# Performance work log

Measured on AMD Instinct MI355X. Metric: run time of the kernel, lower is better.

## Reference

```python
import jax, jax.numpy as jnp
import numpy as np

B, S, D = 16, 1024, 512
N_LAYERS = 3


def setup_inputs() -> dict:
    key = jax.random.key(0)
    ks = jax.random.split(key, 8)
    sc = 0.02  # small init scale keeps gates in a sane range
    return {
        "inputs": jax.random.normal(ks[0], (B, S, D), jnp.float32),
        "h0": jax.random.normal(ks[1], (N_LAYERS, B, D), jnp.float32),
        # GRU params, PyTorch layout: gates ordered (r, z, n), weight [3D, D]
        "w_ih": jax.random.normal(ks[2], (N_LAYERS, 3 * D, D), jnp.float32) * sc,
        "w_hh": jax.random.normal(ks[3], (N_LAYERS, 3 * D, D), jnp.float32) * sc,
        "b_ih": jnp.zeros((N_LAYERS, 3 * D), jnp.float32),
        "b_hh": jnp.zeros((N_LAYERS, 3 * D), jnp.float32),
        "ln0_g": jnp.ones((D,), jnp.float32),
        "ln0_b": jnp.zeros((D,), jnp.float32),
        "ln1_g": jnp.ones((D,), jnp.float32),
        "ln1_b": jnp.zeros((D,), jnp.float32),
        "w1": jax.random.normal(ks[4], (D, 4 * D), jnp.float32) * sc,
        "b1": jnp.zeros((4 * D,), jnp.float32),
        "w2": jax.random.normal(ks[5], (4 * D, D), jnp.float32) * sc,
        "b2": jnp.zeros((D,), jnp.float32),
    }


def _layer_norm(x, g, b, eps=1e-5):
    mu = jnp.mean(x, axis=-1, keepdims=True)
    var = jnp.var(x, axis=-1, keepdims=True)
    return (x - mu) * jax.lax.rsqrt(var + eps) * g + b


def _gru_stack(x, h0, w_ih, w_hh, b_ih, b_hh):
    # x: [S, B, D] time-major; PyTorch GRU math, gate order (r, z, n).
    for l in range(N_LAYERS):
        # precompute input projections for all timesteps (batched GEMM)
        gi = jnp.einsum('sbd,gd->sbg', x, w_ih[l]) + b_ih[l]  # [S, B, 3D]
        w_hh_l_T = w_hh[l].T
        b_hh_l = b_hh[l]

        def step(h, gi_t):
            gh = h @ w_hh_l_T + b_hh_l                       # [B, 3D]
            i_r, i_z, i_n = jnp.split(gi_t, 3, axis=-1)
            h_r, h_z, h_n = jnp.split(gh, 3, axis=-1)
            r = jax.nn.sigmoid(i_r + h_r)
            z = jax.nn.sigmoid(i_z + h_z)
            n = jnp.tanh(i_n + r * h_n)
            h_new = (1.0 - z) * n + z * h
            return h_new, h_new

        _, x = jax.lax.scan(step, h0[l], gi)                 # x: [S, B, D]
    return x


def reference(inputs, h0, w_ih, w_hh, b_ih, b_hh,
              ln0_g, ln0_b, ln1_g, ln1_b, w1, b1, w2, b2):
    # inputs: [B, S, D] -> time-major [S, B, D]
    x = _layer_norm(jnp.transpose(inputs, (1, 0, 2)), ln0_g, ln0_b)
    h = _gru_stack(x, h0, w_ih, w_hh, b_ih, b_hh)            # [S, B, D]
    out = inputs + jnp.transpose(h, (1, 0, 2))               # residual 1 (dropout=identity, eval)
    y = _layer_norm(out, ln1_g, ln1_b)
    ffn = jax.nn.gelu(y @ w1 + b1, approximate=False) @ w2 + b2
    return out + ffn                                          # residual 2
```

## Files before the change

kernel.cpp:

```cpp
#include <hip/hip_runtime.h>
#include <hip/hip_bf16.h>

typedef unsigned short u16;
typedef unsigned int   u32;
typedef unsigned long long u64;
typedef __attribute__((ext_vector_type(8))) short short8;
typedef __attribute__((ext_vector_type(4))) float f32x4;

__device__ __forceinline__ float bf2f(u16 u) {
  union { u32 i; float f; } v; v.i = ((u32)u) << 16; return v.f;
}
__device__ __forceinline__ u16 f2bf(float f) {
  union { float f; u32 i; } v; v.f = f;
  return (u16)((v.i + 0x7FFFu + ((v.i >> 16) & 1u)) >> 16);
}

typedef const __attribute__((address_space(1))) u32* gas_t;
typedef __attribute__((address_space(3)))       u32* las_t;
__device__ __forceinline__ void gld16(const void* g, void* l) {
  __builtin_amdgcn_global_load_lds((gas_t)g, (las_t)l, 16, 0, 0);
}

__global__ __launch_bounds__(256) void cast_kernel(const float* __restrict__ src,
                                                   u16* __restrict__ dst, int n) {
  int i = (blockIdx.x * 256 + threadIdx.x) * 4;
  if (i >= n) return;
  float4 v = *(const float4*)(src + i);
  uint2 o;
  o.x = (u32)f2bf(v.x) | ((u32)f2bf(v.y) << 16);
  o.y = (u32)f2bf(v.z) | ((u32)f2bf(v.w) << 16);
  *(uint2*)(dst + i) = o;
}

__global__ __launch_bounds__(256) void tcast_kernel(const float* __restrict__ src,
                                                    u16* __restrict__ dst, int R, int C) {
  __shared__ u16 tile[32][33];
  int c0 = blockIdx.x * 32, r0 = blockIdx.y * 32;
  for (int dy = threadIdx.y; dy < 32; dy += 8)
    tile[dy][threadIdx.x] = f2bf(src[(size_t)(r0 + dy) * C + c0 + threadIdx.x]);
  __syncthreads();
  for (int dy = threadIdx.y; dy < 32; dy += 8)
    dst[(size_t)(c0 + dy) * R + r0 + threadIdx.x] = tile[threadIdx.x][dy];
}

__global__ __launch_bounds__(256) void hprep_kernel(const float* __restrict__ h0,
                                                    u64* __restrict__ hbuf) {
  int l = blockIdx.x;
  const float* h = h0 + l * 8192;
  u64* buf = hbuf + (size_t)l * 2 * 4096;
  for (int idx = threadIdx.x; idx < 4096; idx += 256) {
    int row = idx >> 8, wl = idx & 255;
    int d0 = wl * 2;
    u64 p0 = f2bf(h[row * 512 + d0]);
    u64 p1 = f2bf(h[row * 512 + d0 + 1]);
    buf[idx] = p0 | (p1 << 32);
  }
}

__global__ __launch_bounds__(256) void ln0_kernel(const float* __restrict__ in,
                                                  const float* __restrict__ g,
                                                  const float* __restrict__ be,
                                                  u16* __restrict__ xout) {
  int m = blockIdx.x;
  int b = m >> 10, s = m & 1023;
  int i = threadIdx.x * 2;
  float2 v = *(const float2*)(in + (size_t)m * 512 + i);
  float sum = v.x + v.y, sq = v.x * v.x + v.y * v.y;
  for (int o = 32; o > 0; o >>= 1) { sum += __shfl_down(sum, o); sq += __shfl_down(sq, o); }
  __shared__ float red[10];
  int w = threadIdx.x >> 6, lane = threadIdx.x & 63;
  if (!lane) { red[w] = sum; red[w + 4] = sq; }
  __syncthreads();
  if (threadIdx.x == 0) {
    sum = red[0] + red[1] + red[2] + red[3];
    sq  = red[4] + red[5] + red[6] + red[7];
    float mu = sum * (1.f / 512.f), var = sq * (1.f / 512.f) - mu * mu;
    red[8] = mu; red[9] = rsqrtf(var + 1e-5f);
  }
  __syncthreads();
  float mu = red[8], rs = red[9];
  u32 o0 = (u32)f2bf((v.x - mu) * rs * g[i] + be[i]) |
           ((u32)f2bf((v.y - mu) * rs * g[i + 1] + be[i + 1]) << 16);
  *(u32*)(xout + (size_t)(s * 16 + b) * 512 + i) = o0;
}

__global__ __launch_bounds__(256) void resid_ln1_kernel(const float* __restrict__ in,
                                                        const u16* __restrict__ hrec,
                                                        const float* __restrict__ g,
                                                        const float* __restrict__ be,
                                                        float* __restrict__ outf,
                                                        u16* __restrict__ y) {
  int m = blockIdx.x;
  int b = m >> 10, s = m & 1023;
  int i = threadIdx.x * 2;
  float2 v = *(const float2*)(in + (size_t)m * 512 + i);
  u32 hu = *(const u32*)(hrec + (size_t)(s * 16 + b) * 512 + i);
  v.x += bf2f((u16)(hu & 0xffff));
  v.y += bf2f((u16)(hu >> 16));
  *(float2*)(outf + (size_t)m * 512 + i) = v;
  float sum = v.x + v.y, sq = v.x * v.x + v.y * v.y;
  for (int o = 32; o > 0; o >>= 1) { sum += __shfl_down(sum, o); sq += __shfl_down(sq, o); }
  __shared__ float red[10];
  int w = threadIdx.x >> 6, lane = threadIdx.x & 63;
  if (!lane) { red[w] = sum; red[w + 4] = sq; }
  __syncthreads();
  if (threadIdx.x == 0) {
    sum = red[0] + red[1] + red[2] + red[3];
    sq  = red[4] + red[5] + red[6] + red[7];
    float mu = sum * (1.f / 512.f), var = sq * (1.f / 512.f) - mu * mu;
    red[8] = mu; red[9] = rsqrtf(var + 1e-5f);
  }
  __syncthreads();
  float mu = red[8], rs = red[9];
  u32 o0 = (u32)f2bf((v.x - mu) * rs * g[i] + be[i]) |
           ((u32)f2bf((v.y - mu) * rs * g[i + 1] + be[i + 1]) << 16);
  *(u32*)(y + (size_t)m * 512 + i) = o0;
}

template <int EPI>
__global__ __launch_bounds__(256, 2)
void gemm_bt(const u16* __restrict__ A, const u16* __restrict__ Bt,
             void* __restrict__ Out, const float* __restrict__ bias,
             const float* __restrict__ resid, int M, int N, int K) {
  __shared__ u16 As[128 * 64];
  __shared__ u16 Bs[128 * 64];
  const int bn = blockIdx.x, bm = blockIdx.y;
  const int tid = threadIdx.x;
  const int w = tid >> 6, lane = tid & 63;
  const int wr = w >> 1, wc = w & 1;
  const int col = lane & 15, kg = lane >> 4;
  const int l8 = lane >> 3, l7 = lane & 7;
  f32x4 acc[4][4];
#pragma unroll
  for (int i = 0; i < 4; ++i)
#pragma unroll
    for (int j = 0; j < 4; ++j) acc[i][j] = (f32x4){0.f, 0.f, 0.f, 0.f};

  for (int k0 = 0; k0 < K; k0 += 64) {
    __syncthreads();
#pragma unroll
    for (int i = 0; i < 4; ++i) {
      int q = w * 4 + i;
      int row = q * 8 + l8;
      int cswz = (l7 * 16) ^ ((row & 7) << 4);
      gld16((const char*)A + ((size_t)(bm * 128 + row) * K + k0) * 2 + cswz,
            (char*)As + q * 1024);
      gld16((const char*)Bt + ((size_t)(bn * 128 + row) * K + k0) * 2 + cswz,
            (char*)Bs + q * 1024);
    }
    asm volatile("s_waitcnt vmcnt(0)" ::: "memory");
    __syncthreads();
#pragma unroll
    for (int kc = 0; kc < 2; ++kc) {
      short8 af[4], bfr[4];
      int cb = kc * 64 + kg * 16;
#pragma unroll
      for (int mi = 0; mi < 4; ++mi) {
        int r = wr * 64 + mi * 16 + col;
        af[mi] = *(const short8*)((const char*)As + r * 128 + (cb ^ ((r & 7) << 4)));
      }
#pragma unroll
      for (int ni = 0; ni < 4; ++ni) {
        int r = wc * 64 + ni * 16 + col;
        bfr[ni] = *(const short8*)((const char*)Bs + r * 128 + (cb ^ ((r & 7) << 4)));
      }
#pragma unroll
      for (int mi = 0; mi < 4; ++mi)
#pragma unroll
        for (int ni = 0; ni < 4; ++ni)
          acc[mi][ni] = __builtin_amdgcn_mfma_f32_16x16x32_bf16(af[mi], bfr[ni], acc[mi][ni], 0, 0, 0);
    }
  }
#pragma unroll
  for (int ni = 0; ni < 4; ++ni) {
    int gn = bn * 128 + wc * 64 + ni * 16 + col;
    float bv = bias ? bias[gn] : 0.f;
#pragma unroll
    for (int mi = 0; mi < 4; ++mi) {
      int gmb = bm * 128 + wr * 64 + mi * 16 + kg * 4;
#pragma unroll
      for (int j = 0; j < 4; ++j) {
        float v = acc[mi][ni][j] + bv;
        size_t idx = (size_t)(gmb + j) * N + gn;
        if (EPI == 0) {
          ((u16*)Out)[idx] = f2bf(v);
        } else if (EPI == 1) {
          float gel = 0.5f * v * (1.f + erff(v * 0.7071067811865476f));
          ((u16*)Out)[idx] = f2bf(gel);
        } else {
          ((float*)Out)[idx] = v + resid[idx];
        }
      }
    }
  }
}

__device__ __forceinline__ void gather_poll(const u64* __restrict__ plane, u32 want,
                                            int w, int lane, u16* __restrict__ lds) {
  const u64 TM = 0xFFFF0000FFFF0000ULL;
  const u64 ex = ((u64)want << 16) | ((u64)want << 48);
  u64 v[16];
#pragma unroll
  for (int r = 0; r < 4; ++r)
#pragma unroll
    for (int q = 0; q < 4; ++q)
      v[r * 4 + q] = __hip_atomic_load(plane + (size_t)(w * 4 + r) * 256 + lane * 4 + q,
                                       __ATOMIC_RELAXED, __HIP_MEMORY_SCOPE_AGENT);
  for (;;) {
    bool ok = true;
#pragma unroll
    for (int i = 0; i < 16; ++i) ok &= ((v[i] ^ ex) & TM) == 0;
    if (ok) break;
    __builtin_amdgcn_s_sleep(1);
#pragma unroll
    for (int i = 0; i < 16; ++i)
      if (((v[i] ^ ex) & TM) != 0)
        v[i] = __hip_atomic_load(plane + (size_t)(w * 4 + (i >> 2)) * 256 + lane * 4 + (i & 3),
                                 __ATOMIC_RELAXED, __HIP_MEMORY_SCOPE_AGENT);
  }
#pragma unroll
  for (int r = 0; r < 4; ++r) {
    int row = w * 4 + r;
    uint4 pk;
    pk.x = ((u32)v[r * 4 + 0] & 0xFFFFu) | ((u32)(v[r * 4 + 0] >> 32) << 16);
    pk.y = ((u32)v[r * 4 + 1] & 0xFFFFu) | ((u32)(v[r * 4 + 1] >> 32) << 16);
    pk.z = ((u32)v[r * 4 + 2] & 0xFFFFu) | ((u32)(v[r * 4 + 2] >> 32) << 16);
    pk.w = ((u32)v[r * 4 + 3] & 0xFFFFu) | ((u32)(v[r * 4 + 3] >> 32) << 16);
    *(uint4*)((char*)lds + row * 1024 + ((lane * 16) ^ ((row & 7) << 4))) = pk;
  }
}

__global__ __launch_bounds__(256, 1)
void rec3_kernel(const u16* __restrict__ gib, const u16* __restrict__ whhb,
                 const u16* __restrict__ wihb, const float* __restrict__ bih,
                 const float* __restrict__ bhh, const float* __restrict__ h0,
                 u64* __restrict__ hpl, u64* __restrict__ xr,
                 u64* __restrict__ gip, u16* __restrict__ xout) {
  const int res = blockIdx.x & 7, grp = blockIdx.x >> 3;
  if (res > 4) return;
  __shared__ u16 hs[16 * 512];
  const int tid = threadIdx.x;
  const int w = tid >> 6, lane = tid & 63;
  const int col = lane & 15, kg = lane >> 4;
  const u64 TM = 0xFFFF0000FFFF0000ULL;

  if (res >= 3) {
    const int l = res - 2, k = grp;
    const int d = k * 64 + w * 16 + col;
    const u16* wih = wihb + (size_t)l * 1536 * 512;
    short8 wi0[16], wi1[16], wi2[16];
    {
      const u16* r0 = wih + (size_t)(0 * 512 + d) * 512;
      const u16* r1 = wih + (size_t)(1 * 512 + d) * 512;
      const u16* r2 = wih + (size_t)(2 * 512 + d) * 512;
#pragma unroll
      for (int kc = 0; kc < 16; ++kc) {
        wi0[kc] = *(const short8*)(r0 + kc * 32 + kg * 8);
        wi1[kc] = *(const short8*)(r1 + kc * 32 + kg * 8);
        wi2[kc] = *(const short8*)(r2 + kc * 32 + kg * 8);
      }
    }
    const float bi0 = bih[l * 1536 + d], bi1 = bih[l * 1536 + 512 + d],
                bi2 = bih[l * 1536 + 1024 + d];
    const u64* upx = xr + (size_t)(l - 1) * 8 * 4096;
    u64* gout = gip + (size_t)(l - 1) * 4 * 12288;
    const u64* hpc = hpl + (size_t)l * 2 * 4096;
    u64 bpv = 0;

    for (int t = 1; t <= 1024; ++t) {
      gather_poll(upx + (size_t)(t & 7) * 4096, (u32)t, w, lane, hs);
      __syncthreads();
      f32x4 ar = {0.f, 0.f, 0.f, 0.f}, az = ar, an = ar;
#pragma unroll
      for (int kc = 0; kc < 16; ++kc) {
        int cb = kc * 64 + kg * 16;
        short8 a = *(const short8*)((const char*)hs + col * 1024 + (cb ^ ((col & 7) << 4)));
        ar = __builtin_amdgcn_mfma_f32_16x16x32_bf16(a, wi0[kc], ar, 0, 0, 0);
        az = __builtin_amdgcn_mfma_f32_16x16x32_bf16(a, wi1[kc], az, 0, 0, 0);
        an = __builtin_amdgcn_mfma_f32_16x16x32_bf16(a, wi2[kc], an, 0, 0, 0);
      }
      if (t > 4) {
        u32 need = (u32)(t - 4);
        u32 ctag = (u32)(bpv >> 16) & 0xFFFFu;
        while (ctag < need) {
          __builtin_amdgcn_s_sleep(8);
          bpv = __hip_atomic_load(hpc + (size_t)(need & 1) * 4096 + k * 32,
                                  __ATOMIC_RELAXED, __HIP_MEMORY_SCOPE_AGENT);
          ctag = (u32)(bpv >> 16) & 0xFFFFu;
        }
      }
      {
        const u32 tgl = (u32)t << 16;
        u64* slot = gout + (size_t)(t & 3) * 12288 + (size_t)k * 1536;
#pragma unroll
        for (int g = 0; g < 3; ++g) {
          f32x4 a = (g == 0) ? ar : ((g == 1) ? az : an);
          float bg = (g == 0) ? bi0 : ((g == 1) ? bi1 : bi2);
#pragma unroll
          for (int jh = 0; jh < 2; ++jh) {
            u32 lo = (u32)f2bf(a[2 * jh] + bg) | tgl;
            u32 hi = (u32)f2bf(a[2 * jh + 1] + bg) | tgl;
            __hip_atomic_store(slot + (size_t)(g * 64 + w * 16 + col) * 8 + kg * 2 + jh,
                               (u64)lo | ((u64)hi << 32),
                               __ATOMIC_RELAXED, __HIP_MEMORY_SCOPE_AGENT);
          }
        }
      }
      if (t >= 4)
        bpv = __hip_atomic_load(hpc + (size_t)((t - 3) & 1) * 4096 + k * 32,
                                __ATOMIC_RELAXED, __HIP_MEMORY_SCOPE_AGENT);
      __syncthreads();
    }
    return;
  }

  const int l = res, blk = grp;
  const int d = blk * 64 + w * 16 + col;
  const u16* whh = whhb + (size_t)l * 1536 * 512;
  short8 wh0[16], wh1[16], wh2[16];
  {
    const u16* r0 = whh + (size_t)(0 * 512 + d) * 512;
    const u16* r1 = whh + (size_t)(1 * 512 + d) * 512;
    const u16* r2 = whh + (size_t)(2 * 512 + d) * 512;
#pragma unroll
    for (int kc = 0; kc < 16; ++kc) {
      wh0[kc] = *(const short8*)(r0 + kc * 32 + kg * 8);
      wh1[kc] = *(const short8*)(r1 + kc * 32 + kg * 8);
      wh2[kc] = *(const short8*)(r2 + kc * 32 + kg * 8);
    }
  }
  const float bh0 = bhh[l * 1536 + d], bh1 = bhh[l * 1536 + 512 + d],
              bh2 = bhh[l * 1536 + 1024 + d];
  float hprev[4];
#pragma unroll
  for (int j = 0; j < 4; ++j) hprev[j] = h0[l * 8192 + (kg * 4 + j) * 512 + d];

  u64* ownp = hpl + (size_t)l * 2 * 4096;
  u64* dnx = xr + (size_t)l * 8 * 4096;
  const u64* gin = gip + (size_t)(l - 1) * 4 * 12288;
  const u64* gchk = gip + (size_t)l * 4 * 12288;
  const bool ev = !(col & 1);
  u64 bp8 = 0;

  for (int t = 1; t <= 1024; ++t) {
    float gir[3][4];
    u64 gv[6];
    if (l == 0) {
#pragma unroll
      for (int gte = 0; gte < 3; ++gte)
#pragma unroll
        for (int j = 0; j < 4; ++j)
          gir[gte][j] = bf2f(gib[((size_t)(t - 1) * 16 + kg * 4 + j) * 1536 + gte * 512 + d]);
    } else {
      const u64* gs = gin + (size_t)(t & 3) * 12288 + (size_t)blk * 1536;
#pragma unroll
      for (int g = 0; g < 3; ++g)
#pragma unroll
        for (int jh = 0; jh < 2; ++jh)
          gv[g * 2 + jh] = __hip_atomic_load(gs + (size_t)(g * 64 + w * 16 + col) * 8 + kg * 2 + jh,
                                             __ATOMIC_RELAXED, __HIP_MEMORY_SCOPE_AGENT);
    }

    gather_poll(ownp + (size_t)((t - 1) & 1) * 4096, (u32)(t - 1), w, lane, hs);

    if (l > 0) {
      const u64 exg = ((u64)t << 16) | ((u64)t << 48);
      const u64* gs = gin + (size_t)(t & 3) * 12288 + (size_t)blk * 1536;
      for (;;) {
        bool ok = true;
#pragma unroll
        for (int i = 0; i < 6; ++i) ok &= ((gv[i] ^ exg) & TM) == 0;
        if (ok) break;
        __builtin_amdgcn_s_sleep(1);
#pragma unroll
        for (int g = 0; g < 3; ++g)
#pragma unroll
          for (int jh = 0; jh < 2; ++jh)
            if (((gv[g * 2 + jh] ^ exg) & TM) != 0)
              gv[g * 2 + jh] = __hip_atomic_load(gs + (size_t)(g * 64 + w * 16 + col) * 8 + kg * 2 + jh,
                                                 __ATOMIC_RELAXED, __HIP_MEMORY_SCOPE_AGENT);
      }
#pragma unroll
      for (int g = 0; g < 3; ++g)
#pragma unroll
        for (int jh = 0; jh < 2; ++jh) {
          gir[g][2 * jh]     = bf2f((u16)gv[g * 2 + jh]);
          gir[g][2 * jh + 1] = bf2f((u16)(gv[g * 2 + jh] >> 32));
        }
    }
    __syncthreads();

    f32x4 ar = {0.f, 0.f, 0.f, 0.f}, az = ar, an = ar;
#pragma unroll
    for (int kc = 0; kc < 16; ++kc) {
      int cb = kc * 64 + kg * 16;
      short8 a = *(const short8*)((const char*)hs + col * 1024 + (cb ^ ((col & 7) << 4)));
      ar = __builtin_amdgcn_mfma_f32_16x16x32_bf16(a, wh0[kc], ar, 0, 0, 0);
      az = __builtin_amdgcn_mfma_f32_16x16x32_bf16(a, wh1[kc], az, 0, 0, 0);
      an = __builtin_amdgcn_mfma_f32_16x16x32_bf16(a, wh2[kc], an, 0, 0, 0);
    }
    u32 po[4];
#pragma unroll
    for (int j = 0; j < 4; ++j) {
      float rg = 1.f / (1.f + expf(-(gir[0][j] + ar[j] + bh0)));
      float zg = 1.f / (1.f + expf(-(gir[1][j] + az[j] + bh1)));
      float ng = tanhf(gir[2][j] + rg * (an[j] + bh2));
      float hn = (1.f - zg) * ng + zg * hprev[j];
      hprev[j] = hn;
      po[j] = (u32)f2bf(hn);
    }

    {
      const u32 tg = (u32)t << 16;
      u32 pn[4];
#pragma unroll
      for (int j = 0; j < 4; ++j) pn[j] = (u32)__shfl_xor((int)po[j], 1);
      int j0 = ev ? 0 : 2;
      u64 wd[2]; int wi_[2];
#pragma unroll
      for (int jj = 0; jj < 2; ++jj) {
        int j = j0 + jj;
        u32 lo = (ev ? po[j] : pn[j]) | tg;
        u32 hi = (ev ? pn[j] : po[j]) | tg;
        int row = kg * 4 + j;
        wd[jj] = (u64)lo | ((u64)hi << 32);
        wi_[jj] = row * 256 + blk * 32 + w * 8 + (col >> 1);
      }
      u64* op = ownp + (size_t)(t & 1) * 4096;
#pragma unroll
      for (int jj = 0; jj < 2; ++jj)
        __hip_atomic_store(op + wi_[jj], wd[jj], __ATOMIC_RELAXED, __HIP_MEMORY_SCOPE_AGENT);

      if (l < 2) {
        if (t > 8) {
          u32 need = (u32)(t - 8);
          for (;;) {
            u32 tg8 = (lane < 8) ? (u32)((bp8 >> 16) & 0xFFFFu) : 0xFFFFu;
            if (__all(tg8 >= need)) break;
            __builtin_amdgcn_s_sleep(8);
            if (lane < 8)
              bp8 = __hip_atomic_load(gchk + (size_t)(need & 3) * 12288 + (size_t)lane * 1536,
                                      __ATOMIC_RELAXED, __HIP_MEMORY_SCOPE_AGENT);
          }
        }
        u64* xp = dnx + (size_t)(t & 7) * 4096;
#pragma unroll
        for (int jj = 0; jj < 2; ++jj)
          __hip_atomic_store(xp + wi_[jj], wd[jj], __ATOMIC_RELAXED, __HIP_MEMORY_SCOPE_AGENT);
        if (t >= 8 && lane < 8)
          bp8 = __hip_atomic_load(gchk + (size_t)((t - 7) & 3) * 12288 + (size_t)lane * 1536,
                                  __ATOMIC_RELAXED, __HIP_MEMORY_SCOPE_AGENT);
      } else {
        u32 pr[4], qr[4];
#pragma unroll
        for (int j = 0; j < 4; ++j) {
          pr[j] = ev ? (po[j] | (pn[j] << 16)) : (pn[j] | (po[j] << 16));
          qr[j] = (u32)__shfl_xor((int)pr[j], 2);
        }
        int jx = col & 3;
        u64 raw = ((col & 2) == 0) ? ((u64)pr[jx] | ((u64)qr[jx] << 32))
                                   : ((u64)qr[jx] | ((u64)pr[jx] << 32));
        int row = kg * 4 + jx;
        *(u64*)(xout + ((size_t)(t - 1) * 16 + row) * 512 + blk * 64 + w * 16 + (col & ~3)) = raw;
      }
    }
    __syncthreads();
  }
}

extern "C" void kernel_launch(void* const* d_in, const int* in_sizes, int n_in,
                              void* d_out, int out_size, void* d_ws, size_t ws_size,
                              hipStream_t stream) {
  const float* inp = (const float*)d_in[0];
  const float* h0  = (const float*)d_in[1];
  const float* wih = (const float*)d_in[2];
  const float* whh = (const float*)d_in[3];
  const float* bih = (const float*)d_in[4];
  const float* bhh = (const float*)d_in[5];
  const float* g0  = (const float*)d_in[6];
  const float* be0 = (const float*)d_in[7];
  const float* g1  = (const float*)d_in[8];
  const float* be1 = (const float*)d_in[9];
  const float* w1  = (const float*)d_in[10];
  const float* b1  = (const float*)d_in[11];
  const float* w2  = (const float*)d_in[12];
  const float* b2  = (const float*)d_in[13];
  float* out = (float*)d_out;

  char* p = (char*)d_ws;
  auto alloc = [&](size_t bytes) {
    char* r = p;
    p += (bytes + 255) & ~(size_t)255;
    return r;
  };
  u16* xa    = (u16*)alloc(16384ull * 512 * 2);
  u16* xb    = (u16*)alloc(16384ull * 512 * 2);
  u16* gib   = (u16*)alloc(16384ull * 1536 * 2);
  u16* mid   = (u16*)alloc(16384ull * 2048 * 2);
  float* outf = (float*)alloc(16384ull * 512 * 4);
  u16* wihb  = (u16*)alloc(3ull * 1536 * 512 * 2);
  u16* whhb  = (u16*)alloc(3ull * 1536 * 512 * 2);
  u16* w1t   = (u16*)alloc(2048ull * 512 * 2);
  u16* w2t   = (u16*)alloc(512ull * 2048 * 2);
  u64* hbuf  = (u64*)alloc(3ull * 2 * 4096 * 8);
  u64* xr    = (u64*)alloc(2ull * 8 * 4096 * 8);
  u64* gip   = (u64*)alloc(2ull * 4 * 12288 * 8);

  hipMemsetAsync(hbuf, 0, 3ull * 2 * 4096 * 8, stream);
  hipMemsetAsync(xr,   0, 2ull * 8 * 4096 * 8, stream);
  hipMemsetAsync(gip,  0, 2ull * 4 * 12288 * 8, stream);
  cast_kernel<<<(3 * 1536 * 512) / 1024, 256, 0, stream>>>(wih, wihb, 3 * 1536 * 512);
  cast_kernel<<<(3 * 1536 * 512) / 1024, 256, 0, stream>>>(whh, whhb, 3 * 1536 * 512);
  hprep_kernel<<<3, 256, 0, stream>>>(h0, hbuf);
  tcast_kernel<<<dim3(2048 / 32, 512 / 32), dim3(32, 8), 0, stream>>>(w1, w1t, 512, 2048);
  tcast_kernel<<<dim3(512 / 32, 2048 / 32), dim3(32, 8), 0, stream>>>(w2, w2t, 2048, 512);
  ln0_kernel<<<16384, 256, 0, stream>>>(inp, g0, be0, xa);

  gemm_bt<0><<<dim3(12, 128), 256, 0, stream>>>(xa, wihb, (void*)gib, bih, nullptr,
                                                16384, 1536, 512);
  rec3_kernel<<<64, 256, 0, stream>>>(gib, whhb, wihb, bih, bhh, h0, hbuf, xr, gip, xb);

  resid_ln1_kernel<<<16384, 256, 0, stream>>>(inp, xb, g1, be1, outf, xa);
  gemm_bt<1><<<dim3(16, 128), 256, 0, stream>>>(xa, w1t, (void*)mid, b1, nullptr,
                                                16384, 2048, 512);
  gemm_bt<2><<<dim3(4, 128), 256, 0, stream>>>(mid, w2t, (void*)out, b2, outf,
                                               16384, 512, 2048);
}
```

Baseline: 4.960 ms.

## Prefetch next-step flag loads across barrier and bound spin loops with watchdog

In the persistent GRU recurrence kernel, the input-projection blocks now issue the next timestep's x-plane atomic loads before the end-of-step barrier, and the hidden blocks prefetch the next step's gate inputs the same way. This hides polling latency behind the barrier and the following work. __syncthreads is replaced by an inline s_waitcnt lgkmcnt(0) plus s_barrier, so vector memory loads can stay outstanding across the barrier. Spin loops get a watchdog bound (WDMAX), which could produce silently wrong results if the bound is ever hit.

```diff
diff --git a/kernel.cpp b/kernel.cpp
--- a/kernel.cpp
+++ b/kernel.cpp
@@ -7,6 +7,8 @@
 typedef __attribute__((ext_vector_type(8))) short short8;
 typedef __attribute__((ext_vector_type(4))) float f32x4;
 
+#define WDMAX (1 << 17)
+
 __device__ __forceinline__ float bf2f(u16 u) {
   union { u32 i; float f; } v; v.i = ((u32)u) << 16; return v.f;
 }
@@ -20,6 +22,8 @@
 __device__ __forceinline__ void gld16(const void* g, void* l) {
   __builtin_amdgcn_global_load_lds((gas_t)g, (las_t)l, 16, 0, 0);
 }
+
+#define WG_BARRIER() asm volatile("s_waitcnt lgkmcnt(0)\n\ts_barrier" ::: "memory")
 
 __global__ __launch_bounds__(256) void cast_kernel(const float* __restrict__ src,
                                                    u16* __restrict__ dst, int n) {
@@ -206,7 +210,7 @@
     for (int q = 0; q < 4; ++q)
       v[r * 4 + q] = __hip_atomic_load(plane + (size_t)(w * 4 + r) * 256 + lane * 4 + q,
                                        __ATOMIC_RELAXED, __HIP_MEMORY_SCOPE_AGENT);
-  for (;;) {
+  for (int wd = 0; wd < WDMAX; ++wd) {
     bool ok = true;
 #pragma unroll
     for (int i = 0; i < 16; ++i) ok &= ((v[i] ^ ex) & TM) == 0;
@@ -266,10 +270,46 @@
     u64* gout = gip + (size_t)(l - 1) * 4 * 12288;
     const u64* hpc = hpl + (size_t)l * 2 * 4096;
     u64 bpv = 0;
-
+    u64 xv[16];
+    {
+      const u64* pl = upx + 1 * 4096;
+#pragma unroll
+      for (int r = 0; r < 4; ++r)
+#pragma unroll
+        for (int q = 0; q < 4; ++q)
+          xv[r * 4 + q] = __hip_atomic_load(pl + (size_t)(w * 4 + r) * 256 + lane * 4 + q,
+                                            __ATOMIC_RELAXED, __HIP_MEMORY_SCOPE_AGENT);
+    }
     for (int t = 1; t <= 1024; ++t) {
-      gather_poll(upx + (size_t)(t & 7) * 4096, (u32)t, w, lane, hs);
-      __syncthreads();
+      const u64* pl = upx + (size_t)(t & 7) * 4096;
+      const u64 ex = ((u64)t << 16) | ((u64)t << 48);
+      for (int wd = 0; wd < WDMAX; ++wd) {
+        bool ok = true;
+#pragma unroll
+        for (int i = 0; i < 16; ++i) ok &= ((xv[i] ^ ex) & TM) == 0;
+        if (ok) break;
+        __builtin_amdgcn_s_sleep(1);
+#pragma unroll
+        for (int r = 0; r < 4; ++r)
+#pragma unroll
+          for (int q = 0; q < 4; ++q)
+            if (((xv[r * 4 + q] ^ ex) & TM) != 0)
+              xv[r * 4 + q] = __hip_atomic_load(pl + (size_t)(w * 4 + r) * 256 + lane * 4 + q,
+                                                __ATOMIC_RELAXED, __HIP_MEMORY_SCOPE_AGENT);
+      }
+      {
+#pragma unroll
+        for (int r = 0; r < 4; ++r) {
+          int row = w * 4 + r;
+          uint4 pk;
+          pk.x = ((u32)xv[r*4+0] & 0xFFFFu) | ((u32)(xv[r*4+0] >> 32) << 16);
+          pk.y = ((u32)xv[r*4+1] & 0xFFFFu) | ((u32)(xv[r*4+1] >> 32) << 16);
+          pk.z = ((u32)xv[r*4+2] & 0xFFFFu) | ((u32)(xv[r*4+2] >> 32) << 16);
+          pk.w = ((u32)xv[r*4+3] & 0xFFFFu) | ((u32)(xv[r*4+3] >> 32) << 16);
+          *(uint4*)((char*)hs + row * 1024 + ((lane * 16) ^ ((row & 7) << 4))) = pk;
+        }
+      }
+      WG_BARRIER();
       f32x4 ar = {0.f, 0.f, 0.f, 0.f}, az = ar, an = ar;
 #pragma unroll
       for (int kc = 0; kc < 16; ++kc) {
@@ -282,7 +322,7 @@
       if (t > 4) {
         u32 need = (u32)(t - 4);
         u32 ctag = (u32)(bpv >> 16) & 0xFFFFu;
-        while (ctag < need) {
+        for (int wd = 0; wd < WDMAX && ctag < need; ++wd) {
           __builtin_amdgcn_s_sleep(8);
           bpv = __hip_atomic_load(hpc + (size_t)(need & 1) * 4096 + k * 32,
                                   __ATOMIC_RELAXED, __HIP_MEMORY_SCOPE_AGENT);
@@ -309,7 +349,16 @@
       if (t >= 4)
         bpv = __hip_atomic_load(hpc + (size_t)((t - 3) & 1) * 4096 + k * 32,
                                 __ATOMIC_RELAXED, __HIP_MEMORY_SCOPE_AGENT);
-      __syncthreads();
+      if (t < 1024) {
+        const u64* np = upx + (size_t)((t + 1) & 7) * 4096;
+#pragma unroll
+        for (int r = 0; r < 4; ++r)
+#pragma unroll
+          for (int q = 0; q < 4; ++q)
+            xv[r * 4 + q] = __hip_atomic_load(np + (size_t)(w * 4 + r) * 256 + lane * 4 + q,
+                                              __ATOMIC_RELAXED, __HIP_MEMORY_SCOPE_AGENT);
+      }
+      WG_BARRIER();
     }
     return;
   }
@@ -341,32 +390,22 @@
   const u64* gchk = gip + (size_t)l * 4 * 12288;
   const bool ev = !(col & 1);
   u64 bp8 = 0;
+  u64 gv[6] = {0, 0, 0, 0, 0, 0};
 
   for (int t = 1; t <= 1024; ++t) {
     float gir[3][4];
-    u64 gv[6];
     if (l == 0) {
 #pragma unroll
       for (int gte = 0; gte < 3; ++gte)
 #pragma unroll
         for (int j = 0; j < 4; ++j)
           gir[gte][j] = bf2f(gib[((size_t)(t - 1) * 16 + kg * 4 + j) * 1536 + gte * 512 + d]);
-    } else {
+    }
+    gather_poll(ownp + (size_t)((t - 1) & 1) * 4096, (u32)(t - 1), w, lane, hs);
+    if (l > 0) {
       const u64* gs = gin + (size_t)(t & 3) * 12288 + (size_t)blk * 1536;
-#pragma unroll
-      for (int g = 0; g < 3; ++g)
-#pragma unroll
-        for (int jh = 0; jh < 2; ++jh)
-          gv[g * 2 + jh] = __hip_atomic_load(gs + (size_t)(g * 64 + w * 16 + col) * 8 + kg * 2 + jh,
-                                             __ATOMIC_RELAXED, __HIP_MEMORY_SCOPE_AGENT);
-    }
-
-    gather_poll(ownp + (size_t)((t - 1) & 1) * 4096, (u32)(t - 1), w, lane, hs);
-
-    if (l > 0) {
       const u64 exg = ((u64)t << 16) | ((u64)t << 48);
-      const u64* gs = gin + (size_t)(t & 3) * 12288 + (size_t)blk * 1536;
-      for (;;) {
+      for (int wd = 0; wd < WDMAX; ++wd) {
         bool ok = true;
 #pragma unroll
         for (int i = 0; i < 6; ++i) ok &= ((gv[i] ^ exg) & TM) == 0;
@@ -388,8 +427,7 @@
           gir[g][2 * jh + 1] = bf2f((u16)(gv[g * 2 + jh] >> 32));
         }
     }
-    __syncthreads();
-
+    WG_BARRIER();
     f32x4 ar = {0.f, 0.f, 0.f, 0.f}, az = ar, an = ar;
 #pragma unroll
     for (int kc = 0; kc < 16; ++kc) {
@@ -409,32 +447,31 @@
       hprev[j] = hn;
       po[j] = (u32)f2bf(hn);
     }
-
     {
       const u32 tg = (u32)t << 16;
       u32 pn[4];
 #pragma unroll
       for (int j = 0; j < 4; ++j) pn[j] = (u32)__shfl_xor((int)po[j], 1);
       int j0 = ev ? 0 : 2;
-      u64 wd[2]; int wi_[2];
+      u64 wd_[2]; int wi_[2];
 #pragma unroll
       for (int jj = 0; jj < 2; ++jj) {
         int j = j0 + jj;
         u32 lo = (ev ? po[j] : pn[j]) | tg;
         u32 hi = (ev ? pn[j] : po[j]) | tg;
         int row = kg * 4 + j;
-        wd[jj] = (u64)lo | ((u64)hi << 32);
+        wd_[jj] = (u64)lo | ((u64)hi << 32);
         wi_[jj] = row * 256 + blk * 32 + w * 8 + (col >> 1);
       }
       u64* op = ownp + (size_t)(t & 1) * 4096;
 #pragma unroll
       for (int jj = 0; jj < 2; ++jj)
-        __hip_atomic_store(op + wi_[jj], wd[jj], __ATOMIC_RELAXED, __HIP_MEMORY_SCOPE_AGENT);
+        __hip_atomic_store(op + wi_[jj], wd_[jj], __ATOMIC_RELAXED, __HIP_MEMORY_SCOPE_AGENT);
 
       if (l < 2) {
         if (t > 8) {
           u32 need = (u32)(t - 8);
-          for (;;) {
+          for (int wd = 0; wd < WDMAX; ++wd) {
             u32 tg8 = (lane < 8) ? (u32)((bp8 >> 16) & 0xFFFFu) : 0xFFFFu;
             if (__all(tg8 >= need)) break;
             __builtin_amdgcn_s_sleep(8);
@@ -446,7 +483,7 @@
         u64* xp = dnx + (size_t)(t & 7) * 4096;
 #pragma unroll
         for (int jj = 0; jj < 2; ++jj)
-          __hip_atomic_store(xp + wi_[jj], wd[jj], __ATOMIC_RELAXED, __HIP_MEMORY_SCOPE_AGENT);
+          __hip_atomic_store(xp + wi_[jj], wd_[jj], __ATOMIC_RELAXED, __HIP_MEMORY_SCOPE_AGENT);
         if (t >= 8 && lane < 8)
           bp8 = __hip_atomic_load(gchk + (size_t)((t - 7) & 3) * 12288 + (size_t)lane * 1536,
                                   __ATOMIC_RELAXED, __HIP_MEMORY_SCOPE_AGENT);
@@ -464,7 +501,16 @@
         *(u64*)(xout + ((size_t)(t - 1) * 16 + row) * 512 + blk * 64 + w * 16 + (col & ~3)) = raw;
       }
     }
-    __syncthreads();
+    if (l > 0 && t < 1024) {
+      const u64* gs2 = gin + (size_t)((t + 1) & 3) * 12288 + (size_t)blk * 1536;
+#pragma unroll
+      for (int g = 0; g < 3; ++g)
+#pragma unroll
+        for (int jh = 0; jh < 2; ++jh)
+          gv[g * 2 + jh] = __hip_atomic_load(gs2 + (size_t)(g * 64 + w * 16 + col) * 8 + kg * 2 + jh,
+                                             __ATOMIC_RELAXED, __HIP_MEMORY_SCOPE_AGENT);
+    }
+    WG_BARRIER();
   }
 }
 
@@ -506,9 +552,9 @@
   u64* xr    = (u64*)alloc(2ull * 8 * 4096 * 8);
   u64* gip   = (u64*)alloc(2ull * 4 * 12288 * 8);
 
-  hipMemsetAsync(hbuf, 0, 3ull * 2 * 4096 * 8, stream);
-  hipMemsetAsync(xr,   0, 2ull * 8 * 4096 * 8, stream);
-  hipMemsetAsync(gip,  0, 2ull * 4 * 12288 * 8, stream);
+  (void)hipMemsetAsync(hbuf, 0, 3ull * 2 * 4096 * 8, stream);
+  (void)hipMemsetAsync(xr,   0, 2ull * 8 * 4096 * 8, stream);
+  (void)hipMemsetAsync(gip,  0, 2ull * 4 * 12288 * 8, stream);
   cast_kernel<<<(3 * 1536 * 512) / 1024, 256, 0, stream>>>(wih, wihb, 3 * 1536 * 512);
   cast_kernel<<<(3 * 1536 * 512) / 1024, 256, 0, stream>>>(whh, whhb, 3 * 1536 * 512);
   hprep_kernel<<<3, 256, 0, stream>>>(h0, hbuf);
```

New measurement: 4.982 ms. Within noise of the previous version (+0.4%).
